# Kernel tuning notes

Measured on AMD Instinct MI355X. Metric: run time of the kernel, lower is better.

Reference implementation:

```python
import jax, jax.numpy as jnp
import numpy as np

T, B, IN, H, L = 512, 64, 1024, 1024, 2


def setup_inputs() -> dict:
    key = jax.random.key(0)
    ks = jax.random.split(key, 9)
    stdv = 1.0 / np.sqrt(H)
    u = lambda k, shape: jax.random.uniform(k, shape, jnp.float32, -stdv, stdv)
    return {
        "x": jax.random.normal(ks[0], (T, B, IN), jnp.float32),
        "h0": jnp.zeros((L, B, H), jnp.float32),
        "w_ih_l0": u(ks[1], (3 * H, IN)),
        "w_hh_l0": u(ks[2], (3 * H, H)),
        "b_ih_l0": u(ks[3], (3 * H,)),
        "b_hh_l0": u(ks[4], (3 * H,)),
        "w_ih_l1": u(ks[5], (3 * H, H)),
        "w_hh_l1": u(ks[6], (3 * H, H)),
        "b_ih_l1": u(ks[7], (3 * H,)),
        "b_hh_l1": u(ks[8], (3 * H,)),
    }


def _gru_layer(x, h, w_ih, w_hh, b_ih, b_hh):
    # Precompute input-side gates for all timesteps: [T, B, 3H]
    gx = jnp.einsum('tbi,gi->tbg', x, w_ih) + b_ih

    def step(h_prev, gx_t):
        gh = h_prev @ w_hh.T + b_hh  # [B, 3H]
        gxr, gxz, gxn = jnp.split(gx_t, 3, axis=-1)
        ghr, ghz, ghn = jnp.split(gh, 3, axis=-1)
        r = jax.nn.sigmoid(gxr + ghr)
        z = jax.nn.sigmoid(gxz + ghz)
        n = jnp.tanh(gxn + r * ghn)
        h_new = n + z * (h_prev - n)
        return h_new, h_new

    h_last, ys = jax.lax.scan(step, h, gx)
    return ys, h_last


def reference(x, h0, w_ih_l0, w_hh_l0, b_ih_l0, b_hh_l0,
              w_ih_l1, w_hh_l1, b_ih_l1, b_hh_l1):
    y0, hn0 = _gru_layer(x, h0[0], w_ih_l0, w_hh_l0, b_ih_l0, b_hh_l0)
    y1, hn1 = _gru_layer(y0, h0[1], w_ih_l1, w_hh_l1, b_ih_l1, b_hh_l1)
    return y1, jnp.stack([hn0, hn1], axis=0)
```

## Files before the change

kernel.cpp:

```cpp
#include <hip/hip_runtime.h>
#include <hip/hip_bf16.h>
#include <math.h>

#define T_STEPS 512
#define BATCH   64
#define HID     1024
#define G3      3072
#define BH      (BATCH * HID)

typedef __attribute__((ext_vector_type(8))) short          bf16x8;
typedef __attribute__((ext_vector_type(8))) unsigned short u16x8;
typedef __attribute__((ext_vector_type(4))) float          f32x4;
typedef unsigned long long u64;

__device__ inline unsigned short f2bf(float f) {
    __hip_bfloat16 h = __float2bfloat16(f);
    return *reinterpret_cast<unsigned short*>(&h);
}

__device__ inline bf16x8 load_h8(const unsigned short* p) {
    u64 lo = __hip_atomic_load((const u64*)p,       __ATOMIC_RELAXED, __HIP_MEMORY_SCOPE_AGENT);
    u64 hi = __hip_atomic_load((const u64*)(p + 4), __ATOMIC_RELAXED, __HIP_MEMORY_SCOPE_AGENT);
    union { u64 q[2]; bf16x8 v; } u;
    u.q[0] = lo; u.q[1] = hi;
    return u.v;
}

__device__ inline float fast_sigmoid(float x) {
    return __builtin_amdgcn_rcpf(1.f + __expf(-x));
}
__device__ inline float fast_tanh(float x) {
    float e = __expf(-2.f * fabsf(x));
    float t = (1.f - e) * __builtin_amdgcn_rcpf(1.f + e);
    return copysignf(t, x);
}

__global__ void cvt_f32_bf16(const float* __restrict__ src,
                             unsigned short* __restrict__ dst, int n)
{
    int i = (blockIdx.x * blockDim.x + threadIdx.x) * 4;
    if (i + 3 < n) {
        float4 v = *(const float4*)(src + i);
        ushort4 o;
        o.x = f2bf(v.x); o.y = f2bf(v.y); o.z = f2bf(v.z); o.w = f2bf(v.w);
        *(ushort4*)(dst + i) = o;
    }
}

__global__ __launch_bounds__(256) void gemm_gx_bf16(
    const float* __restrict__ A, const unsigned short* __restrict__ Wbf,
    const float* __restrict__ bias, float* __restrict__ C, int M)
{
    __shared__ unsigned short As[128][72];
    __shared__ unsigned short Bs[128][72];
    const int tid = threadIdx.x;
    const int l  = tid & 63;
    const int w  = tid >> 6;
    const int wm = w >> 1, wn = w & 1;
    const int m0 = blockIdx.y * 128, n0 = blockIdx.x * 128;
    const int lr = l & 15, lk = (l >> 4) * 8;

    f32x4 acc[4][4] = {};

    const int arow = tid >> 4, acol = (tid & 15) * 4;
    const int brow = tid >> 3, bcol = (tid & 7) * 8;

    for (int k0 = 0; k0 < 1024; k0 += 64) {
        float4 av[8];
        #pragma unroll
        for (int r = 0; r < 8; ++r)
            av[r] = *(const float4*)(A + (size_t)(m0 + r * 16 + arow) * 1024 + k0 + acol);
        u16x8 bv[4];
        #pragma unroll
        for (int r = 0; r < 4; ++r)
            bv[r] = *(const u16x8*)(Wbf + (size_t)(n0 + r * 32 + brow) * 1024 + k0 + bcol);

        __syncthreads();
        #pragma unroll
        for (int r = 0; r < 8; ++r) {
            ushort4 o;
            o.x = f2bf(av[r].x); o.y = f2bf(av[r].y);
            o.z = f2bf(av[r].z); o.w = f2bf(av[r].w);
            *(ushort4*)&As[r * 16 + arow][acol] = o;
        }
        #pragma unroll
        for (int r = 0; r < 4; ++r)
            *(u16x8*)&Bs[r * 32 + brow][bcol] = bv[r];
        __syncthreads();

        #pragma unroll
        for (int kk = 0; kk < 2; ++kk) {
            bf16x8 af[4], bfr[4];
            #pragma unroll
            for (int i = 0; i < 4; ++i)
                af[i] = *(const bf16x8*)&As[wm * 64 + i * 16 + lr][kk * 32 + lk];
            #pragma unroll
            for (int j = 0; j < 4; ++j)
                bfr[j] = *(const bf16x8*)&Bs[wn * 64 + j * 16 + lr][kk * 32 + lk];
            #pragma unroll
            for (int i = 0; i < 4; ++i)
                #pragma unroll
                for (int j = 0; j < 4; ++j)
                    acc[i][j] = __builtin_amdgcn_mfma_f32_16x16x32_bf16(
                        af[i], bfr[j], acc[i][j], 0, 0, 0);
        }
    }

    #pragma unroll
    for (int j = 0; j < 4; ++j) {
        const int col = n0 + wn * 64 + j * 16 + lr;
        const float bv = bias[col];
        #pragma unroll
        for (int i = 0; i < 4; ++i) {
            const int rb = m0 + wm * 64 + i * 16 + (l >> 4) * 4;
            #pragma unroll
            for (int r = 0; r < 4; ++r)
                C[(size_t)(rb + r) * G3 + col] = acc[i][j][r] + bv;
        }
    }
}

__global__ __launch_bounds__(256, 1) void gru_persist(
    const float* __restrict__ gx,
    unsigned short* __restrict__ hbf,
    const float* __restrict__ hprev0,
    const unsigned short* __restrict__ whh,
    const float* __restrict__ bhh,
    float* __restrict__ y_all,
    float* __restrict__ hn_dst,
    unsigned int* __restrict__ flags,
    int step_base, int t0, int tc)
{
    __shared__ float red[4][64][13];

    const int tid = threadIdx.x;
    const int bid = blockIdx.x;
    const int jt = bid & 63;
    const int bg = bid >> 6;
    const int l   = tid & 63;
    const int ks  = tid >> 6;
    const int lr  = l & 15;
    const int lgrp = l >> 4;

    const unsigned short* hpb = hbf + (size_t)(bg * 16 + lr) * HID + ks * 256 + lgrp * 8;
    const unsigned short* wr  = whh + (size_t)(jt * 16 + lr) * HID + ks * 256 + lgrp * 8;
    const unsigned short* wz  = wr + (size_t)HID * HID;
    const unsigned short* wn  = wz + (size_t)HID * HID;

    bf16x8 wvr[8], wvz[8], wvn[8];
    #pragma unroll
    for (int kc = 0; kc < 8; ++kc) {
        wvr[kc] = *(const bf16x8*)(wr + kc * 32);
        wvz[kc] = *(const bf16x8*)(wz + kc * 32);
        wvn[kc] = *(const bf16x8*)(wn + kc * 32);
    }

    const int q  = tid >> 6;
    const int fl = tid & 63;
    const int j  = jt * 16 + (fl & 15);
    const int b  = bg * 16 + 4 * (fl >> 4) + q;
    const float brc = bhh[j], bzc = bhh[HID + j], bnc = bhh[2 * HID + j];
    float hreg = hprev0[(size_t)b * HID + j];

    float gxr = gx[(size_t)b * G3 + j];
    float gxz = gx[(size_t)b * G3 + HID + j];
    float gxn = gx[(size_t)b * G3 + 2 * HID + j];

    for (int ts = 0; ts < tc; ++ts) {
        const int t = t0 + ts;
        const size_t coff = (size_t)(t & 1) * BH;
        const size_t noff = (size_t)((t + 1) & 1) * BH;
        const unsigned int stamp = (unsigned int)(step_base + ts + 1);

        f32x4 ar = {0.f, 0.f, 0.f, 0.f};
        f32x4 az = {0.f, 0.f, 0.f, 0.f};
        f32x4 an = {0.f, 0.f, 0.f, 0.f};
        #pragma unroll
        for (int kc = 0; kc < 8; ++kc) {
            bf16x8 a = load_h8(hpb + coff + kc * 32);
            ar = __builtin_amdgcn_mfma_f32_16x16x32_bf16(a, wvr[kc], ar, 0, 0, 0);
            az = __builtin_amdgcn_mfma_f32_16x16x32_bf16(a, wvz[kc], az, 0, 0, 0);
            an = __builtin_amdgcn_mfma_f32_16x16x32_bf16(a, wvn[kc], an, 0, 0, 0);
        }
        #pragma unroll
        for (int i = 0; i < 4; ++i) {
            red[ks][l][i]     = ar[i];
            red[ks][l][4 + i] = az[i];
            red[ks][l][8 + i] = an[i];
        }
        __syncthreads();

        float sr = 0.f, sz = 0.f, sn = 0.f;
        #pragma unroll
        for (int s = 0; s < 4; ++s) {
            sr += red[s][fl][q];
            sz += red[s][fl][4 + q];
            sn += red[s][fl][8 + q];
        }
        const float rg = fast_sigmoid(gxr + sr + brc);
        const float zg = fast_sigmoid(gxz + sz + bzc);
        const float ng = fast_tanh(gxn + rg * (sn + bnc));
        hreg = ng + zg * (hreg - ng);

        unsigned int myu = (unsigned int)f2bf(hreg);
        unsigned int pu  = __shfl_xor(myu, 1);
        if (!(fl & 1))
            __hip_atomic_store((unsigned int*)(hbf + noff + (size_t)b * HID + j),
                               myu | (pu << 16),
                               __ATOMIC_RELAXED, __HIP_MEMORY_SCOPE_AGENT);

        __syncthreads();
        if (tid == 0)
            __hip_atomic_store(&flags[bg * 64 + jt], stamp,
                               __ATOMIC_RELAXED, __HIP_MEMORY_SCOPE_AGENT);

        y_all[(size_t)t * BH + (size_t)b * HID + j] = hreg;
        if (t == T_STEPS - 1)
            hn_dst[(size_t)b * HID + j] = hreg;
        const int tsn = (ts + 1 < tc) ? ts + 1 : ts;
        const float* gxp = gx + (size_t)tsn * BATCH * G3;
        const float ngxr = gxp[(size_t)b * G3 + j];
        const float ngxz = gxp[(size_t)b * G3 + HID + j];
        const float ngxn = gxp[(size_t)b * G3 + 2 * HID + j];

        if (tid < 64) {
            for (;;) {
                unsigned int f = __hip_atomic_load(&flags[bg * 64 + tid],
                                                   __ATOMIC_RELAXED,
                                                   __HIP_MEMORY_SCOPE_AGENT);
                if (__ballot(f >= stamp) == ~0ull) break;
                __builtin_amdgcn_s_sleep(1);
            }
        }
        __syncthreads();
        gxr = ngxr; gxz = ngxz; gxn = ngxn;
    }
}

extern "C" void kernel_launch(void* const* d_in, const int* in_sizes, int n_in,
                              void* d_out, int out_size, void* d_ws, size_t ws_size,
                              hipStream_t stream)
{
    const float* x    = (const float*)d_in[0];
    const float* h0   = (const float*)d_in[1];
    const float* wih[2] = {(const float*)d_in[2], (const float*)d_in[6]};
    const float* whh[2] = {(const float*)d_in[3], (const float*)d_in[7]};
    const float* bih[2] = {(const float*)d_in[4], (const float*)d_in[8]};
    const float* bhh[2] = {(const float*)d_in[5], (const float*)d_in[9]};

    float* out = (float*)d_out;
    float* y   = out;
    float* hn  = out + (size_t)T_STEPS * BH;

    const size_t WSZ = (size_t)G3 * HID;
    unsigned short* wsu = (unsigned short*)d_ws;
    unsigned short* whh_bf[2] = {wsu, wsu + WSZ};
    unsigned short* wih_bf[2] = {wsu + 2 * WSZ, wsu + 3 * WSZ};
    unsigned short* hbf = wsu + 4 * WSZ;
    unsigned int* flags = (unsigned int*)(wsu + 4 * WSZ + 2 * (size_t)BH);
    const size_t FLAG_N = 4 * 64;
    float* gx = (float*)((char*)flags + FLAG_N * sizeof(unsigned int));
    const size_t fixed_bytes = (4 * WSZ + 2 * (size_t)BH) * 2 + FLAG_N * 4;
    const size_t gx_bytes = ws_size > fixed_bytes ? ws_size - fixed_bytes : 0;

    int TC = 512;
    while (TC > 2 && (size_t)TC * BATCH * G3 * 4 > gx_bytes) TC >>= 1;

    hipMemsetAsync(flags, 0, FLAG_N * sizeof(unsigned int), stream);

    for (int layer = 0; layer < 2; ++layer) {
        cvt_f32_bf16<<<(int)(WSZ / 1024), 256, 0, stream>>>(whh[layer], whh_bf[layer], (int)WSZ);
        cvt_f32_bf16<<<(int)(WSZ / 1024), 256, 0, stream>>>(wih[layer], wih_bf[layer], (int)WSZ);
    }

    for (int layer = 0; layer < 2; ++layer) {
        const float* A_all = (layer == 0) ? x : y;
        const float* hinit = h0 + (size_t)layer * BH;

        cvt_f32_bf16<<<BH / 1024, 256, 0, stream>>>(hinit, hbf, BH);

        for (int c0 = 0; c0 < T_STEPS; c0 += TC) {
            dim3 ggrid(G3 / 128, TC * BATCH / 128);
            gemm_gx_bf16<<<ggrid, 256, 0, stream>>>(
                A_all + (size_t)c0 * BH, wih_bf[layer], bih[layer],
                gx, TC * BATCH);

            const float* gxp = gx;
            const float* hprev0 = (c0 == 0) ? hinit : (y + (size_t)(c0 - 1) * BH);
            const unsigned short* whhp = whh_bf[layer];
            const float* bhhp = bhh[layer];
            float* yp = y;
            float* hnp = hn + (size_t)layer * BH;
            unsigned short* hbfp = hbf;
            unsigned int* flp = flags;
            int sb = layer * T_STEPS + c0;
            int t0v = c0, tcv = TC;
            void* kargs[] = {(void*)&gxp, (void*)&hbfp, (void*)&hprev0,
                             (void*)&whhp, (void*)&bhhp, (void*)&yp,
                             (void*)&hnp, (void*)&flp,
                             (void*)&sb, (void*)&t0v, (void*)&tcv};
            hipLaunchCooperativeKernel((const void*)gru_persist,
                                       dim3(256), dim3(256), kargs, 0, stream);
        }
    }
}
```

Baseline: 5.703 ms.

## Use per-wave flags and per-wave polling for recurrent step synchronisation

Replaces the per-block flag and single-wave polling plus block barrier with per-wave flags: each wave publishes its own stamp after its h stores drain, and each wave polls only the 64 flags it needs before its MFMA loop. This removes one block-wide barrier and the end-of-step wait, letting waves start the next step as soon as their inputs are ready. It also moves the gx load to the top of each step instead of prefetching it, and quadruples the flag array. The risk is more polling traffic and a subtle ordering hazard if the vmcnt wait does not make the stores visible before the flag.

```diff
diff --git a/kernel.cpp b/kernel.cpp
--- a/kernel.cpp
+++ b/kernel.cpp
@@ -162,15 +162,28 @@
     const float brc = bhh[j], bzc = bhh[HID + j], bnc = bhh[2 * HID + j];
     float hreg = hprev0[(size_t)b * HID + j];
 
-    float gxr = gx[(size_t)b * G3 + j];
-    float gxz = gx[(size_t)b * G3 + HID + j];
-    float gxn = gx[(size_t)b * G3 + 2 * HID + j];
+    unsigned int* myflag = flags + bg * 256 + jt * 4 + ks;
+    const unsigned int* pollf = flags + bg * 256 + ks * 64 + l;
 
     for (int ts = 0; ts < tc; ++ts) {
         const int t = t0 + ts;
         const size_t coff = (size_t)(t & 1) * BH;
         const size_t noff = (size_t)((t + 1) & 1) * BH;
-        const unsigned int stamp = (unsigned int)(step_base + ts + 1);
+        const unsigned int need  = (unsigned int)(step_base + ts);
+        const unsigned int stamp = need + 1;
+
+        const float* gx_t = gx + (size_t)ts * BATCH * G3;
+        const float gxr = gx_t[(size_t)b * G3 + j];
+        const float gxz = gx_t[(size_t)b * G3 + HID + j];
+        const float gxn = gx_t[(size_t)b * G3 + 2 * HID + j];
+
+        for (;;) {
+            unsigned int f = __hip_atomic_load(pollf, __ATOMIC_RELAXED,
+                                               __HIP_MEMORY_SCOPE_AGENT);
+            if (__ballot(f < need) == 0ull) break;
+            __builtin_amdgcn_s_sleep(1);
+        }
+        __builtin_amdgcn_sched_barrier(0);
 
         f32x4 ar = {0.f, 0.f, 0.f, 0.f};
         f32x4 az = {0.f, 0.f, 0.f, 0.f};
@@ -197,6 +210,8 @@
             sz += red[s][fl][4 + q];
             sn += red[s][fl][8 + q];
         }
+        __syncthreads();
+
         const float rg = fast_sigmoid(gxr + sr + brc);
         const float zg = fast_sigmoid(gxz + sz + bzc);
         const float ng = fast_tanh(gxn + rg * (sn + bnc));
@@ -209,31 +224,14 @@
                                myu | (pu << 16),
                                __ATOMIC_RELAXED, __HIP_MEMORY_SCOPE_AGENT);
 
-        __syncthreads();
-        if (tid == 0)
-            __hip_atomic_store(&flags[bg * 64 + jt], stamp,
+        asm volatile("s_waitcnt vmcnt(0)" ::: "memory");
+        if (l == 0)
+            __hip_atomic_store(myflag, stamp,
                                __ATOMIC_RELAXED, __HIP_MEMORY_SCOPE_AGENT);
 
         y_all[(size_t)t * BH + (size_t)b * HID + j] = hreg;
         if (t == T_STEPS - 1)
             hn_dst[(size_t)b * HID + j] = hreg;
-        const int tsn = (ts + 1 < tc) ? ts + 1 : ts;
-        const float* gxp = gx + (size_t)tsn * BATCH * G3;
-        const float ngxr = gxp[(size_t)b * G3 + j];
-        const float ngxz = gxp[(size_t)b * G3 + HID + j];
-        const float ngxn = gxp[(size_t)b * G3 + 2 * HID + j];
-
-        if (tid < 64) {
-            for (;;) {
-                unsigned int f = __hip_atomic_load(&flags[bg * 64 + tid],
-                                                   __ATOMIC_RELAXED,
-                                                   __HIP_MEMORY_SCOPE_AGENT);
-                if (__ballot(f >= stamp) == ~0ull) break;
-                __builtin_amdgcn_s_sleep(1);
-            }
-        }
-        __syncthreads();
-        gxr = ngxr; gxz = ngxz; gxn = ngxn;
     }
 }
 
@@ -258,7 +256,7 @@
     unsigned short* wih_bf[2] = {wsu + 2 * WSZ, wsu + 3 * WSZ};
     unsigned short* hbf = wsu + 4 * WSZ;
     unsigned int* flags = (unsigned int*)(wsu + 4 * WSZ + 2 * (size_t)BH);
-    const size_t FLAG_N = 4 * 64;
+    const size_t FLAG_N = 4 * 64 * 4;
     float* gx = (float*)((char*)flags + FLAG_N * sizeof(unsigned int));
     const size_t fixed_bytes = (4 * WSZ + 2 * (size_t)BH) * 2 + FLAG_N * 4;
     const size_t gx_bytes = ws_size > fixed_bytes ? ws_size - fixed_bytes : 0;
```

Result: slower. 8.403 ms (+47.3%).
